# Performance work log

Hardware: AMD Instinct MI355X
Metric: run time of the kernel (lower is better)

The kernel has to match this reference:

```python
import jax, jax.numpy as jnp
import numpy as np

NUM_USERS = 200000
NUM_ITEMS = 100000
EMBED_DIM = 64
NUM_LAYERS = 3
NUM_EDGES = 2000000
BATCH = 16384
EPS = 1e-12


def setup_inputs() -> dict:
    key = jax.random.key(0)
    k1, k2, k3, k4, k5, k6 = jax.random.split(key, 6)
    # xavier_uniform bound for (N, d) embedding: sqrt(6/(N+d))
    bu = float(np.sqrt(6.0 / (NUM_USERS + EMBED_DIM)))
    bi = float(np.sqrt(6.0 / (NUM_ITEMS + EMBED_DIM)))
    user_table = jax.random.uniform(k1, (NUM_USERS, EMBED_DIM), jnp.float32, -bu, bu)
    item_table = jax.random.uniform(k2, (NUM_ITEMS, EMBED_DIM), jnp.float32, -bi, bi)
    u_nodes = jax.random.randint(k3, (NUM_EDGES,), 0, NUM_USERS, dtype=jnp.int64 if jax.config.jax_enable_x64 else jnp.int32)
    i_nodes = jax.random.randint(k4, (NUM_EDGES,), 0, NUM_ITEMS, dtype=u_nodes.dtype)
    edge_index = jnp.stack([u_nodes, i_nodes], axis=0)  # [2, E]
    user_indices = jax.random.randint(k5, (BATCH,), 0, NUM_USERS, dtype=u_nodes.dtype)
    item_indices = jax.random.randint(k6, (BATCH,), 0, NUM_ITEMS, dtype=u_nodes.dtype)
    return {
        "user_table": user_table,
        "item_table": item_table,
        "user_indices": user_indices,
        "item_indices": item_indices,
        "edge_index": edge_index,
    }


def _l2_normalize(x):
    # matches torch F.normalize(p=2, dim=1, eps=1e-12)
    norm = jnp.sqrt(jnp.sum(x * x, axis=1, keepdims=True))
    return x / jnp.maximum(norm, EPS)


def reference(user_table, item_table, user_indices, item_indices, edge_index):
    u_nodes = edge_index[0]
    i_nodes = edge_index[1]
    user_emb = user_table
    item_emb = item_table
    user_sum = user_emb
    item_sum = item_emb
    for _ in range(NUM_LAYERS):
        # scatter-add messages along edges (gather source rows, segment-sum to dest)
        user_agg = jax.ops.segment_sum(item_emb[i_nodes], u_nodes, num_segments=NUM_USERS)
        item_agg = jax.ops.segment_sum(user_emb[u_nodes], i_nodes, num_segments=NUM_ITEMS)
        user_emb = _l2_normalize(user_agg)
        item_emb = _l2_normalize(item_agg)
        user_sum = user_sum + user_emb
        item_sum = item_sum + item_emb
    final_user = user_sum / (NUM_LAYERS + 1)
    final_item = item_sum / (NUM_LAYERS + 1)
    return jnp.sum(final_user[user_indices] * final_item[item_indices], axis=1)
```

## Files before the change

### kernel.cpp

```cpp
#include <hip/hip_runtime.h>
#include <hip/hip_fp16.h>

#define NUM_USERS 200000
#define NUM_ITEMS 100000
#define DIM 64
#define NUM_EDGES 2000000
#define BATCH 16384
#define NUM_LAYERS 3

#define NU64 ((size_t)NUM_USERS * DIM)
#define NI64 ((size_t)NUM_ITEMS * DIM)

#define RU_SHIFT 11
#define RI_SHIFT 10
#define NBU 98
#define NBI 98
#define CAPU 24576
#define CAPI 24576
#define EPB 1024


__global__ void convert_kernel(const float4* __restrict__ ut, const float4* __restrict__ it,
                               uint2* __restrict__ uH, uint2* __restrict__ iH) {
    int idx = blockIdx.x * blockDim.x + threadIdx.x;
    const int n4u = (int)(NU64 / 4), n4i = (int)(NI64 / 4);
    if (idx < n4u) {
        float4 v = ut[idx];
        __half2 h0 = __floats2half2_rn(v.x, v.y);
        __half2 h1 = __floats2half2_rn(v.z, v.w);
        uint2 p; p.x = *(unsigned*)&h0; p.y = *(unsigned*)&h1;
        uH[idx] = p;
    } else if (idx < n4u + n4i) {
        int k = idx - n4u;
        float4 v = it[k];
        __half2 h0 = __floats2half2_rn(v.x, v.y);
        __half2 h1 = __floats2half2_rn(v.z, v.w);
        uint2 p; p.x = *(unsigned*)&h0; p.y = *(unsigned*)&h1;
        iH[k] = p;
    }
}


__global__ void final_dot_kernel(const float* __restrict__ uT, const float* __restrict__ iT,
                                 const __half* __restrict__ uE1, const __half* __restrict__ uE2,
                                 const __half* __restrict__ uE3,
                                 const __half* __restrict__ iE1, const __half* __restrict__ iE2,
                                 const __half* __restrict__ iE3,
                                 const int* __restrict__ u_idx, const int* __restrict__ i_idx,
                                 float* __restrict__ out) {
    int b    = (blockIdx.x * blockDim.x + threadIdx.x) >> 6;
    int lane = threadIdx.x & 63;
    if (b >= BATCH) return;
    int u = u_idx[b];
    int i = i_idx[b];
    size_t uo = (size_t)u * DIM + lane;
    size_t io = (size_t)i * DIM + lane;
    float su = uT[uo] + __half2float(uE1[uo]) + __half2float(uE2[uo]) + __half2float(uE3[uo]);
    float si = iT[io] + __half2float(iE1[io]) + __half2float(iE2[io]) + __half2float(iE3[io]);
    float p = su * si;
    #pragma unroll
    for (int o = 32; o > 0; o >>= 1) p += __shfl_xor(p, o, 64);
    if (lane == 0) out[b] = p * (1.0f / ((NUM_LAYERS + 1) * (NUM_LAYERS + 1)));
}


__global__ void bucket_scatter(const int* __restrict__ un, const int* __restrict__ in_,
                               int* __restrict__ gcurU, int* __restrict__ gcurI,
                               int2* __restrict__ stageU, int2* __restrict__ stageI) {
    __shared__ int cntU[4][NBU], cntI[4][NBI];
    __shared__ int baseU[4][NBU], baseI[4][NBI];
    int t = threadIdx.x;
    int w = t >> 6;
    for (int k = t; k < 4 * NBU; k += 256) ((int*)cntU)[k] = 0;
    for (int k = t; k < 4 * NBI; k += 256) ((int*)cntI)[k] = 0;
    __syncthreads();
    int e0 = blockIdx.x * EPB + t;
    int u[4], it[4], bu[4], bi[4], ru[4], ri[4];
    bool valid[4];
    #pragma unroll
    for (int k = 0; k < 4; ++k) {
        int e = e0 + k * 256;
        valid[k] = (e < NUM_EDGES);
        if (valid[k]) {
            u[k]  = un[e];
            it[k] = in_[e];
            bu[k] = u[k]  >> RU_SHIFT;
            bi[k] = it[k] >> RI_SHIFT;
            ru[k] = atomicAdd(&cntU[w][bu[k]], 1);
            ri[k] = atomicAdd(&cntI[w][bi[k]], 1);
        }
    }
    __syncthreads();
    if (t < NBU) {
        int c0 = cntU[0][t], c1 = cntU[1][t], c2 = cntU[2][t], c3 = cntU[3][t];
        int b = t * CAPU + atomicAdd(&gcurU[t], c0 + c1 + c2 + c3);
        baseU[0][t] = b; baseU[1][t] = b + c0; baseU[2][t] = b + c0 + c1; baseU[3][t] = b + c0 + c1 + c2;
    }
    if (t < NBI) {
        int c0 = cntI[0][t], c1 = cntI[1][t], c2 = cntI[2][t], c3 = cntI[3][t];
        int b = t * CAPI + atomicAdd(&gcurI[t], c0 + c1 + c2 + c3);
        baseI[0][t] = b; baseI[1][t] = b + c0; baseI[2][t] = b + c0 + c1; baseI[3][t] = b + c0 + c1 + c2;
    }
    __syncthreads();
    #pragma unroll
    for (int k = 0; k < 4; ++k) {
        if (valid[k]) {
            stageU[baseU[w][bu[k]] + ru[k]] = make_int2(u[k], it[k]);
            stageI[baseI[w][bi[k]] + ri[k]] = make_int2(it[k], u[k]);
        }
    }
}

__global__ void bucket_place(const int* __restrict__ gcurU, const int* __restrict__ gcurI,
                             const int2* __restrict__ stageU, const int2* __restrict__ stageI,
                             int* __restrict__ u_offs, int* __restrict__ i_offs,
                             int* __restrict__ u_deg, int* __restrict__ i_deg,
                             int* __restrict__ u_adj, int* __restrict__ i_adj) {
    __shared__ int cnt[2048];
    __shared__ int offs_l[2048];
    __shared__ int wsum[1024];
    int b = blockIdx.x, t = threadIdx.x;
    const int2* stage; int* adj; int* offs; int* deg; int lo, range, nrec, bbase;
    if (b < NBU) {
        stage = stageU + (size_t)b * CAPU; adj = u_adj; offs = u_offs; deg = u_deg;
        nrec = gcurU[b]; lo = b << RU_SHIFT; bbase = b * CAPU;
        range = NUM_USERS - lo; if (range > 2048) range = 2048;
    } else {
        int bb = b - NBU;
        stage = stageI + (size_t)bb * CAPI; adj = i_adj; offs = i_offs; deg = i_deg;
        nrec = gcurI[bb]; lo = bb << RI_SHIFT; bbase = bb * CAPI;
        range = NUM_ITEMS - lo; if (range > 1024) range = 1024;
    }
    cnt[t] = 0; cnt[t + 1024] = 0;
    __syncthreads();
    for (int r = t; r < nrec; r += 1024) atomicAdd(&cnt[stage[r].x - lo], 1);
    __syncthreads();
    int c0 = cnt[2 * t], c1 = cnt[2 * t + 1];
    int s = c0 + c1;
    wsum[t] = s;
    __syncthreads();
    for (int off = 1; off < 1024; off <<= 1) {
        int v = (t >= off) ? wsum[t - off] : 0;
        __syncthreads();
        wsum[t] += v;
        __syncthreads();
    }
    int excl = wsum[t] - s;
    offs_l[2 * t] = excl;
    offs_l[2 * t + 1] = excl + c0;
    if (2 * t < range)     { offs[lo + 2 * t]     = bbase + excl;      deg[lo + 2 * t]     = c0; }
    if (2 * t + 1 < range) { offs[lo + 2 * t + 1] = bbase + excl + c0; deg[lo + 2 * t + 1] = c1; }
    cnt[2 * t] = 0; cnt[2 * t + 1] = 0;
    __syncthreads();
    for (int r = t; r < nrec; r += 1024) {
        int2 rec = stage[r];
        int loc = rec.x - lo;
        int p = atomicAdd(&cnt[loc], 1);
        adj[bbase + offs_l[loc] + p] = rec.y;
    }
}

__global__ void pull_norm_kernel(const int* __restrict__ u_offs, const int* __restrict__ u_deg,
                                 const int* __restrict__ u_adj,
                                 const int* __restrict__ i_offs, const int* __restrict__ i_deg,
                                 const int* __restrict__ i_adj,
                                 const __half* __restrict__ uprev, const __half* __restrict__ iprev,
                                 __half* __restrict__ unew, __half* __restrict__ inew) {
    int w    = (blockIdx.x * blockDim.x + threadIdx.x) >> 6;
    int lane = threadIdx.x & 63;
    int half = lane >> 5;
    int l32  = lane & 31;
    const int* offs; const int* deg; const int* adj; const __half* src; __half* demb; int row;
    if (w < NUM_USERS) {
        row = w; offs = u_offs; deg = u_deg; adj = u_adj; src = iprev; demb = unew;
    } else {
        row = w - NUM_USERS;
        if (row >= NUM_ITEMS) return;
        offs = i_offs; deg = i_deg; adj = i_adj; src = uprev; demb = inew;
    }
    int start = offs[row];
    int cnt   = deg[row];
    float ax = 0.0f, ay = 0.0f;
    for (int base = 0; base < cnt; base += 64) {
        int rem = cnt - base;
        if (rem > 64) rem = 64;
        int idx = (lane < rem) ? adj[start + base + lane] : 0;
        int j = 0;
        for (; j + 8 <= rem; j += 8) {
            #pragma unroll
            for (int p = 0; p < 4; ++p) {
                int nb = __shfl(idx, j + 2 * p + half, 64);
                const __half2* srow = (const __half2*)(src + (size_t)nb * DIM);
                float2 v = __half22float2(srow[l32]);
                ax += v.x; ay += v.y;
            }
        }
        for (; j + 2 <= rem; j += 2) {
            int nb = __shfl(idx, j + half, 64);
            const __half2* srow = (const __half2*)(src + (size_t)nb * DIM);
            float2 v = __half22float2(srow[l32]);
            ax += v.x; ay += v.y;
        }
        if (j < rem) {
            int nb = __shfl(idx, j, 64);
            const __half2* srow = (const __half2*)(src + (size_t)nb * DIM);
            float2 v = __half22float2(srow[l32]);
            if (half == 0) { ax += v.x; ay += v.y; }
        }
    }
    ax += __shfl_xor(ax, 32, 64);
    ay += __shfl_xor(ay, 32, 64);
    float ss = ax * ax + ay * ay;
    #pragma unroll
    for (int o = 16; o > 0; o >>= 1) ss += __shfl_xor(ss, o, 64);
    float inv = 1.0f / fmaxf(sqrtf(ss), 1e-12f);
    float nx = ax * inv, ny = ay * inv;
    if (half == 0) {
        ((__half2*)(demb + (size_t)row * DIM))[l32] = __floats2half2_rn(nx, ny);
    }
}


extern "C" void kernel_launch(void* const* d_in, const int* in_sizes, int n_in,
                              void* d_out, int out_size, void* d_ws, size_t ws_size,
                              hipStream_t stream) {
    const float* user_table = (const float*)d_in[0];
    const float* item_table = (const float*)d_in[1];
    const int*   u_idx      = (const int*)d_in[2];
    const int*   i_idx      = (const int*)d_in[3];
    const int*   edges      = (const int*)d_in[4];
    const int*   u_nodes    = edges;
    const int*   i_nodes    = edges + NUM_EDGES;
    float*       out        = (float*)d_out;

    __half* uH0 = (__half*)d_ws;
    __half* uE1 = uH0 + NU64;
    __half* uE2 = uE1 + NU64;
    __half* uE3 = uE2 + NU64;
    __half* iH0 = uE3 + NU64;
    __half* iE1 = iH0 + NI64;
    __half* iE2 = iE1 + NI64;
    __half* iE3 = iE2 + NI64;

    int* ip     = (int*)(iE3 + NI64);
    int* u_offs = ip;
    int* i_offs = u_offs + NUM_USERS;
    int* u_deg  = i_offs + NUM_ITEMS;
    int* i_deg  = u_deg + NUM_USERS;
    int* u_adj  = i_deg + NUM_ITEMS;
    int* i_adj  = u_adj + (size_t)NBU * CAPU;
    int* gcurU  = i_adj + (size_t)NBI * CAPI;
    int* gcurI  = gcurU + NBU;
    int2* stageU = (int2*)(gcurI + NBI);
    int2* stageI = stageU + (size_t)NBU * CAPU;

    {
        int n4 = (int)((NU64 + NI64) / 4);
        convert_kernel<<<(n4 + 255) / 256, 256, 0, stream>>>(
            (const float4*)user_table, (const float4*)item_table,
            (uint2*)uH0, (uint2*)iH0);
    }

    hipMemsetAsync(gcurU, 0, (NBU + NBI) * sizeof(int), stream);

    int nblkA = (NUM_EDGES + EPB - 1) / EPB;
    bucket_scatter<<<nblkA, 256, 0, stream>>>(u_nodes, i_nodes, gcurU, gcurI, stageU, stageI);
    bucket_place<<<NBU + NBI, 1024, 0, stream>>>(gcurU, gcurI, stageU, stageI,
                                                 u_offs, i_offs, u_deg, i_deg, u_adj, i_adj);

    long long waves = (long long)(NUM_USERS + NUM_ITEMS);
    int blocks = (int)((waves * 64 + 255) / 256);
    const __half* uprevs[3] = {uH0, uE1, uE2};
    const __half* iprevs[3] = {iH0, iE1, iE2};
    __half* udsts[3] = {uE1, uE2, uE3};
    __half* idsts[3] = {iE1, iE2, iE3};
    for (int l = 0; l < NUM_LAYERS; ++l) {
        pull_norm_kernel<<<blocks, 256, 0, stream>>>(u_offs, u_deg, u_adj,
                                                     i_offs, i_deg, i_adj,
                                                     uprevs[l], iprevs[l],
                                                     udsts[l], idsts[l]);
    }

    {
        long long tb = (long long)BATCH * 64;
        final_dot_kernel<<<(int)((tb + 255) / 256), 256, 0, stream>>>(
            user_table, item_table, uE1, uE2, uE3, iE1, iE2, iE3, u_idx, i_idx, out);
    }
}
```

Before: 521.4 us.

## Pack staging records into 32-bit words and simplify pull kernel to per-lane scalar gathers

Staging records for CSR construction are packed into a single 32-bit word (local row index in the high bits, neighbor id in the low 18 bits) instead of an int2, halving staging write and read traffic. The pull/normalize kernel is rewritten so that each lane handles one feature of a 64-wide row, with neighbor indices read as wave-uniform scalar loads via readfirstlane. Neighbors are processed four at a time, replacing the half-wave shuffle-based layout. Each gather is now a 2-byte load per lane rather than a 4-byte half2 load, and the per-edge index loads are scalar, which may change memory-level parallelism.

```diff
diff --git a/kernel.cpp b/kernel.cpp
--- a/kernel.cpp
+++ b/kernel.cpp
@@ -18,6 +18,7 @@
 #define CAPU 24576
 #define CAPI 24576
 #define EPB 1024
+#define VMASK 0x3FFFF
 
 
 __global__ void convert_kernel(const float4* __restrict__ ut, const float4* __restrict__ it,
@@ -66,7 +67,7 @@
 
 __global__ void bucket_scatter(const int* __restrict__ un, const int* __restrict__ in_,
                                int* __restrict__ gcurU, int* __restrict__ gcurI,
-                               int2* __restrict__ stageU, int2* __restrict__ stageI) {
+                               unsigned* __restrict__ stageU, unsigned* __restrict__ stageI) {
     __shared__ int cntU[4][NBU], cntI[4][NBI];
     __shared__ int baseU[4][NBU], baseI[4][NBI];
     int t = threadIdx.x;
@@ -105,14 +106,14 @@
     #pragma unroll
     for (int k = 0; k < 4; ++k) {
         if (valid[k]) {
-            stageU[baseU[w][bu[k]] + ru[k]] = make_int2(u[k], it[k]);
-            stageI[baseI[w][bi[k]] + ri[k]] = make_int2(it[k], u[k]);
+            stageU[baseU[w][bu[k]] + ru[k]] = ((unsigned)(u[k]  & ((1 << RU_SHIFT) - 1)) << 18) | (unsigned)it[k];
+            stageI[baseI[w][bi[k]] + ri[k]] = ((unsigned)(it[k] & ((1 << RI_SHIFT) - 1)) << 18) | (unsigned)u[k];
         }
     }
 }
 
 __global__ void bucket_place(const int* __restrict__ gcurU, const int* __restrict__ gcurI,
-                             const int2* __restrict__ stageU, const int2* __restrict__ stageI,
+                             const unsigned* __restrict__ stageU, const unsigned* __restrict__ stageI,
                              int* __restrict__ u_offs, int* __restrict__ i_offs,
                              int* __restrict__ u_deg, int* __restrict__ i_deg,
                              int* __restrict__ u_adj, int* __restrict__ i_adj) {
@@ -120,7 +121,7 @@
     __shared__ int offs_l[2048];
     __shared__ int wsum[1024];
     int b = blockIdx.x, t = threadIdx.x;
-    const int2* stage; int* adj; int* offs; int* deg; int lo, range, nrec, bbase;
+    const unsigned* stage; int* adj; int* offs; int* deg; int lo, range, nrec, bbase;
     if (b < NBU) {
         stage = stageU + (size_t)b * CAPU; adj = u_adj; offs = u_offs; deg = u_deg;
         nrec = gcurU[b]; lo = b << RU_SHIFT; bbase = b * CAPU;
@@ -133,7 +134,7 @@
     }
     cnt[t] = 0; cnt[t + 1024] = 0;
     __syncthreads();
-    for (int r = t; r < nrec; r += 1024) atomicAdd(&cnt[stage[r].x - lo], 1);
+    for (int r = t; r < nrec; r += 1024) atomicAdd(&cnt[stage[r] >> 18], 1);
     __syncthreads();
     int c0 = cnt[2 * t], c1 = cnt[2 * t + 1];
     int s = c0 + c1;
@@ -153,10 +154,10 @@
     cnt[2 * t] = 0; cnt[2 * t + 1] = 0;
     __syncthreads();
     for (int r = t; r < nrec; r += 1024) {
-        int2 rec = stage[r];
-        int loc = rec.x - lo;
+        unsigned rec = stage[r];
+        int loc = (int)(rec >> 18);
         int p = atomicAdd(&cnt[loc], 1);
-        adj[bbase + offs_l[loc] + p] = rec.y;
+        adj[bbase + offs_l[loc] + p] = (int)(rec & VMASK);
     }
 }
 
@@ -168,8 +169,6 @@
                                  __half* __restrict__ unew, __half* __restrict__ inew) {
     int w    = (blockIdx.x * blockDim.x + threadIdx.x) >> 6;
     int lane = threadIdx.x & 63;
-    int half = lane >> 5;
-    int l32  = lane & 31;
     const int* offs; const int* deg; const int* adj; const __half* src; __half* demb; int row;
     if (w < NUM_USERS) {
         row = w; offs = u_offs; deg = u_deg; adj = u_adj; src = iprev; demb = unew;
@@ -178,46 +177,31 @@
         if (row >= NUM_ITEMS) return;
         offs = i_offs; deg = i_deg; adj = i_adj; src = uprev; demb = inew;
     }
-    int start = offs[row];
-    int cnt   = deg[row];
-    float ax = 0.0f, ay = 0.0f;
-    for (int base = 0; base < cnt; base += 64) {
-        int rem = cnt - base;
-        if (rem > 64) rem = 64;
-        int idx = (lane < rem) ? adj[start + base + lane] : 0;
-        int j = 0;
-        for (; j + 8 <= rem; j += 8) {
-            #pragma unroll
-            for (int p = 0; p < 4; ++p) {
-                int nb = __shfl(idx, j + 2 * p + half, 64);
-                const __half2* srow = (const __half2*)(src + (size_t)nb * DIM);
-                float2 v = __half22float2(srow[l32]);
-                ax += v.x; ay += v.y;
-            }
-        }
-        for (; j + 2 <= rem; j += 2) {
-            int nb = __shfl(idx, j + half, 64);
-            const __half2* srow = (const __half2*)(src + (size_t)nb * DIM);
-            float2 v = __half22float2(srow[l32]);
-            ax += v.x; ay += v.y;
-        }
-        if (j < rem) {
-            int nb = __shfl(idx, j, 64);
-            const __half2* srow = (const __half2*)(src + (size_t)nb * DIM);
-            float2 v = __half22float2(srow[l32]);
-            if (half == 0) { ax += v.x; ay += v.y; }
-        }
-    }
-    ax += __shfl_xor(ax, 32, 64);
-    ay += __shfl_xor(ay, 32, 64);
-    float ss = ax * ax + ay * ay;
-    #pragma unroll
-    for (int o = 16; o > 0; o >>= 1) ss += __shfl_xor(ss, o, 64);
+    row = __builtin_amdgcn_readfirstlane(row);
+    int start = __builtin_amdgcn_readfirstlane(offs[row]);
+    int cnt   = __builtin_amdgcn_readfirstlane(deg[row]);
+    float a = 0.0f;
+    int j = 0;
+    for (; j + 4 <= cnt; j += 4) {
+        int n0 = adj[start + j];
+        int n1 = adj[start + j + 1];
+        int n2 = adj[start + j + 2];
+        int n3 = adj[start + j + 3];
+        float v0 = __half2float(src[(size_t)n0 * DIM + lane]);
+        float v1 = __half2float(src[(size_t)n1 * DIM + lane]);
+        float v2 = __half2float(src[(size_t)n2 * DIM + lane]);
+        float v3 = __half2float(src[(size_t)n3 * DIM + lane]);
+        a += (v0 + v1) + (v2 + v3);
+    }
+    for (; j < cnt; ++j) {
+        int nb = adj[start + j];
+        a += __half2float(src[(size_t)nb * DIM + lane]);
+    }
+    float ss = a * a;
+    #pragma unroll
+    for (int o = 32; o > 0; o >>= 1) ss += __shfl_xor(ss, o, 64);
     float inv = 1.0f / fmaxf(sqrtf(ss), 1e-12f);
-    float nx = ax * inv, ny = ay * inv;
-    if (half == 0) {
-        ((__half2*)(demb + (size_t)row * DIM))[l32] = __floats2half2_rn(nx, ny);
-    }
+    demb[(size_t)row * DIM + lane] = __float2half(a * inv);
 }
 
 
@@ -251,8 +235,8 @@
     int* i_adj  = u_adj + (size_t)NBU * CAPU;
     int* gcurU  = i_adj + (size_t)NBI * CAPI;
     int* gcurI  = gcurU + NBU;
-    int2* stageU = (int2*)(gcurI + NBI);
-    int2* stageI = stageU + (size_t)NBU * CAPU;
+    unsigned* stageU = (unsigned*)(gcurI + NBI);
+    unsigned* stageI = stageU + (size_t)NBU * CAPU;
 
     {
         int n4 = (int)((NU64 + NI64) / 4);
```

New measurement: 632.9 us. 1.21x slower.
